# Kernel optimization log

Hardware: AMD Instinct MI355X
Metric: run time of the kernel (lower is better)

## Reference

```python
import jax, jax.numpy as jnp
import numpy as np

B, S, E = 2, 2048, 2048
H, KV, HD = 16, 4, 128  # num_heads, num_kv_heads, head_dim
G = H // KV             # query heads per kv head
ROPE_BASE = 10000.0


def rope_tables(dim, maxlen):
    freqs = 1.0 / ROPE_BASE ** (jnp.arange(0, dim, 2, dtype=jnp.float32) / dim)
    t = jnp.arange(maxlen, dtype=jnp.float32)
    f = jnp.outer(t, freqs)  # (maxlen, dim//2)
    return jnp.cos(f), jnp.sin(f)


def apply_rope(x, cos, sin):
    # x: (..., seq, heads, head_dim); interleaved-pair rotation
    s_len = x.shape[-3]
    c = cos[:s_len][:, None, :]
    s = sin[:s_len][:, None, :]
    x1 = x[..., ::2]
    x2 = x[..., 1::2]
    return jnp.stack([x1 * c - x2 * s, x1 * s + x2 * c], axis=-1).reshape(x.shape)


def setup_inputs() -> dict:
    key = jax.random.key(0)
    kx, kq, kk, kv, ko = jax.random.split(key, 5)
    x = jax.random.normal(kx, (B, S, E), dtype=jnp.float32)
    Wq = jax.random.normal(kq, (E, H * HD), dtype=jnp.float32) * 0.02
    Wk = jax.random.normal(kk, (E, KV * HD), dtype=jnp.float32) * 0.02
    Wv = jax.random.normal(kv, (E, KV * HD), dtype=jnp.float32) * 0.02
    Wo = jax.random.normal(ko, (H * HD, E), dtype=jnp.float32) * 0.02
    mask = jnp.tril(jnp.ones((S, S), dtype=bool))[None, None]  # causal (1,1,S,S)
    return {"x": x, "Wq": Wq, "Wk": Wk, "Wv": Wv, "Wo": Wo, "mask": mask}


def reference(x, Wq, Wk, Wv, Wo, mask):
    b, s, _ = x.shape
    cos, sin = rope_tables(HD, s)
    q = (x @ Wq).reshape(b, s, H, HD)
    k = (x @ Wk).reshape(b, s, KV, HD)
    v = (x @ Wv).reshape(b, s, KV, HD)
    q = apply_rope(q, cos, sin)
    k = apply_rope(k, cos, sin)
    if G > 1:
        k = jnp.repeat(k, G, axis=2)  # (b, s, H, HD)
        v = jnp.repeat(v, G, axis=2)
    q = jnp.transpose(q, (0, 2, 1, 3))  # (b, H, s, HD)
    k = jnp.transpose(k, (0, 2, 1, 3))
    v = jnp.transpose(v, (0, 2, 1, 3))
    scale = jnp.sqrt(jnp.float32(HD)).astype(q.dtype)
    scores = jnp.einsum("bhqd,bhkd->bhqk", q, k) / scale
    scores = jnp.where(mask, scores, jnp.finfo(scores.dtype).min)
    attn = jax.nn.softmax(scores, axis=-1)
    out = jnp.einsum("bhqk,bhkd->bhqd", attn, v)
    out = jnp.transpose(out, (0, 2, 1, 3)).reshape(b, s, H * HD)
    return out @ Wo
```

## Files before the change

### kernel.cpp

```cpp
#include <hip/hip_runtime.h>
#include <hip/hip_bf16.h>
#include <cstdint>

#define B_ 2
#define S_ 2048
#define E_ 2048
#define H_ 16
#define KV_ 4
#define HD_ 128
#define BS_ (B_*S_)
#define QKV_LD 3072
#define SM_SCALE 0.08838834764831845f

typedef __attribute__((ext_vector_type(8))) __bf16 bf16x8;
typedef __attribute__((ext_vector_type(4))) float  floatx4;

__device__ __forceinline__ unsigned short f2bf(float f) {
  union { float f; unsigned u; } v; v.f = f;
  unsigned r = v.u + 0x7fffu + ((v.u >> 16) & 1u);
  return (unsigned short)(r >> 16);
}
__device__ __forceinline__ float bf2f(unsigned short u) {
  union { unsigned u; float f; } v; v.u = ((unsigned)u) << 16; return v.f;
}

__global__ __launch_bounds__(256)
void cvt_bf16(const float* __restrict__ src, unsigned short* __restrict__ dst,
              int rows, int cols, int dld, int doff) {
  int idx = blockIdx.x * 256 + threadIdx.x;
  int n = rows * cols / 4;
  if (idx >= n) return;
  int e = idx * 4;
  int r = e / cols, c = e % cols;
  float4 v = *(const float4*)(src + (size_t)r * cols + c);
  ushort4 o;
  o.x = f2bf(v.x); o.y = f2bf(v.y); o.z = f2bf(v.z); o.w = f2bf(v.w);
  *(ushort4*)(dst + (size_t)r * dld + doff + c) = o;
}

__global__ __launch_bounds__(256)
void rope_kernel(unsigned short* __restrict__ qkv) {
  const int PPR = 1280;
  int idx = blockIdx.x * 256 + threadIdx.x;
  if (idx >= BS_ * PPR) return;
  int row = idx / PPR, p = idx - row * PPR;
  int col = (p < 1024) ? (2 * p) : (2048 + 2 * (p - 1024));
  int d = p & 63;
  int s = row & (S_ - 1);
  float freq = expf(-(float)d * 0.14391156831212787f);
  float ang = (float)s * freq;
  float c = cosf(ang), sn = sinf(ang);
  unsigned short* ptr = qkv + (size_t)row * QKV_LD + col;
  float x1 = bf2f(ptr[0]), x2 = bf2f(ptr[1]);
  ptr[0] = f2bf(x1 * c - x2 * sn);
  ptr[1] = f2bf(x1 * sn + x2 * c);
}

__global__ __launch_bounds__(256)
void vtrans_kernel(const unsigned short* __restrict__ qkv,
                   unsigned short* __restrict__ vt) {
  __shared__ unsigned short tile[64 * 72];
  const int tid = threadIdx.x;
  const int s0 = blockIdx.x * 64;
  const int g = blockIdx.y >> 1;
  const int hh = (blockIdx.y & 1) * 64;
  const int b = g >> 2, kvh = g & 3;
#pragma unroll
  for (int i = 0; i < 2; ++i) {
    int chunk = tid + i * 256;
    int r = chunk >> 3, c = (chunk & 7) * 8;
    uint4 v = *(const uint4*)(qkv + (size_t)(b * S_ + s0 + r) * QKV_LD + 2560 + kvh * HD_ + hh + c);
    *(uint4*)(tile + r * 72 + c) = v;
  }
  __syncthreads();
#pragma unroll
  for (int i = 0; i < 2; ++i) {
    int chunk = tid + i * 256;
    int hdr = chunk >> 3, sc = (chunk & 7) * 8;
    union { unsigned short u[8]; uint4 v; } t;
#pragma unroll
    for (int j = 0; j < 8; ++j) t.u[j] = tile[(sc + j) * 72 + hdr];
    *(uint4*)(vt + (size_t)(g * HD_ + hh + hdr) * S_ + s0 + sc) = t.v;
  }
}

template<bool OUT_BF16>
__global__ __launch_bounds__(256, 2)
void gemm_bf16(const unsigned short* __restrict__ A,
               const unsigned short* __restrict__ Bm,
               void* __restrict__ C, int M, int N, int K) {
  constexpr int ST = 72;
  __shared__ unsigned short Ash[128 * ST];
  __shared__ unsigned short Bt[128 * ST];
  const int tid = threadIdx.x;
  const int lane = tid & 63;
  const int l16 = lane & 15, l4 = lane >> 4;
  const int wave = tid >> 6;
  const int wm = (wave >> 1) * 64, wn = (wave & 1) * 64;
  const int bm = blockIdx.y * 128, bn = blockIdx.x * 128;

  floatx4 acc[4][4] = {};

  for (int kb = 0; kb < K; kb += 32) {
    __syncthreads();
#pragma unroll
    for (int i = 0; i < 2; ++i) {
      int chunk = tid + i * 256;
      int r = chunk >> 2, cc = (chunk & 3) * 8;
      uint4 v = *(const uint4*)(A + (size_t)(bm + r) * K + kb + cc);
      *(uint4*)(Ash + r * ST + cc) = v;
    }
#pragma unroll
    for (int i = 0; i < 2; ++i) {
      int chunk = tid + i * 256;
      int col = chunk & 127, kg = (chunk >> 7) * 8;
      const unsigned short* bp = Bm + (size_t)(kb + kg) * N + bn + col;
      union { unsigned short u[8]; uint4 v; } t;
#pragma unroll
      for (int j = 0; j < 8; ++j) t.u[j] = bp[(size_t)j * N];
      *(uint4*)(Bt + col * ST + kg) = t.v;
    }
    __syncthreads();
    bf16x8 af[4], bf[4];
#pragma unroll
    for (int t = 0; t < 4; ++t)
      af[t] = *(const bf16x8*)(Ash + (wm + t * 16 + l16) * ST + l4 * 8);
#pragma unroll
    for (int t = 0; t < 4; ++t)
      bf[t] = *(const bf16x8*)(Bt + (wn + t * 16 + l16) * ST + l4 * 8);
#pragma unroll
    for (int tm = 0; tm < 4; ++tm)
#pragma unroll
      for (int tn = 0; tn < 4; ++tn)
        acc[tm][tn] = __builtin_amdgcn_mfma_f32_16x16x32_bf16(af[tm], bf[tn], acc[tm][tn], 0, 0, 0);
  }
#pragma unroll
  for (int tm = 0; tm < 4; ++tm)
#pragma unroll
    for (int tn = 0; tn < 4; ++tn)
#pragma unroll
      for (int r = 0; r < 4; ++r) {
        int row = bm + wm + tm * 16 + l4 * 4 + r;
        int col = bn + wn + tn * 16 + l16;
        float v = acc[tm][tn][r];
        if (OUT_BF16) ((unsigned short*)C)[(size_t)row * N + col] = f2bf(v);
        else          ((float*)C)[(size_t)row * N + col] = v;
      }
}

__global__ __launch_bounds__(512, 2)
void gqa_attention(const unsigned short* __restrict__ qkv,
                   const unsigned short* __restrict__ vt,
                   unsigned short* __restrict__ out) {
  constexpr int KST = 136;
  constexpr int VST = 40;
  constexpr int PST = 40;
  __shared__ unsigned short Ksh[32 * KST];
  __shared__ unsigned short Vtsh[128 * VST];
  __shared__ unsigned short Psh[8][16 * PST];

  const int tid = threadIdx.x, lane = tid & 63, wave = tid >> 6;
  const int l16 = lane & 15, l4 = lane >> 4;
  const int g = blockIdx.y, b = g >> 2, kvh = g & 3;
  const int h = kvh * 4 + (wave & 3);
  const int qsub = wave >> 2;
  const int bx = blockIdx.x;

  const int kr = tid >> 4, kc = (tid & 15) * 8;
  const int vr = tid >> 2, vc = (tid & 3) * 8;

  for (int phase = 0; phase < 2; ++phase) {
    const int q0 = phase ? (S_ - 32 - bx * 32) : (bx * 32);
    const int qt = q0 + qsub * 16;

    bf16x8 qf[4];
    {
      const unsigned short* qp = qkv + (size_t)(b * S_ + qt + l16) * QKV_LD + h * HD_;
#pragma unroll
      for (int c = 0; c < 4; ++c)
        qf[c] = *(const bf16x8*)(qp + c * 32 + l4 * 8);
    }

    floatx4 acc[8] = {};
    float mrow[4], lrow[4];
#pragma unroll
    for (int r = 0; r < 4; ++r) { mrow[r] = -3e38f; lrow[r] = 0.f; }

    for (int kb = 0; kb <= q0; kb += 32) {
      __syncthreads();
      {
        uint4 v = *(const uint4*)(qkv + (size_t)(b * S_ + kb + kr) * QKV_LD + 2048 + kvh * HD_ + kc);
        *(uint4*)(Ksh + kr * KST + kc) = v;
      }
      {
        uint4 v = *(const uint4*)(vt + (size_t)(g * HD_ + vr) * S_ + kb + vc);
        *(uint4*)(Vtsh + vr * VST + vc) = v;
      }
      __syncthreads();

      floatx4 sacc[2] = {};
#pragma unroll
      for (int half = 0; half < 2; ++half)
#pragma unroll
        for (int c = 0; c < 4; ++c) {
          bf16x8 kf = *(const bf16x8*)(Ksh + (half * 16 + l16) * KST + c * 32 + l4 * 8);
          sacc[half] = __builtin_amdgcn_mfma_f32_16x16x32_bf16(qf[c], kf, sacc[half], 0, 0, 0);
        }
      float s[2][4];
      if (kb == q0) {
#pragma unroll
        for (int half = 0; half < 2; ++half)
#pragma unroll
          for (int r = 0; r < 4; ++r) {
            int ka = kb + half * 16 + l16;
            int qa = qt + l4 * 4 + r;
            s[half][r] = (ka > qa) ? -3e38f : sacc[half][r] * SM_SCALE;
          }
      } else {
#pragma unroll
        for (int half = 0; half < 2; ++half)
#pragma unroll
          for (int r = 0; r < 4; ++r)
            s[half][r] = sacc[half][r] * SM_SCALE;
      }
      float mx[4];
#pragma unroll
      for (int r = 0; r < 4; ++r) mx[r] = fmaxf(s[0][r], s[1][r]);
#pragma unroll
      for (int off = 1; off < 16; off <<= 1)
#pragma unroll
        for (int r = 0; r < 4; ++r)
          mx[r] = fmaxf(mx[r], __shfl_xor(mx[r], off, 64));
      float mnew[4], alpha[4], ps[4];
#pragma unroll
      for (int r = 0; r < 4; ++r) {
        mnew[r] = fmaxf(mrow[r], mx[r]);
        alpha[r] = __expf(mrow[r] - mnew[r]);
        ps[r] = 0.f;
      }
#pragma unroll
      for (int t = 0; t < 8; ++t)
#pragma unroll
        for (int r = 0; r < 4; ++r)
          acc[t][r] *= alpha[r];
#pragma unroll
      for (int half = 0; half < 2; ++half)
#pragma unroll
        for (int r = 0; r < 4; ++r) {
          float p = __expf(s[half][r] - mnew[r]);
          ps[r] += p;
          Psh[wave][(l4 * 4 + r) * PST + half * 16 + l16] = f2bf(p);
        }
#pragma unroll
      for (int off = 1; off < 16; off <<= 1)
#pragma unroll
        for (int r = 0; r < 4; ++r)
          ps[r] += __shfl_xor(ps[r], off, 64);
#pragma unroll
      for (int r = 0; r < 4; ++r) {
        lrow[r] = lrow[r] * alpha[r] + ps[r];
        mrow[r] = mnew[r];
      }
      bf16x8 pf = *(const bf16x8*)(&Psh[wave][l16 * PST + l4 * 8]);
#pragma unroll
      for (int t = 0; t < 8; ++t) {
        bf16x8 vf = *(const bf16x8*)(Vtsh + (t * 16 + l16) * VST + l4 * 8);
        acc[t] = __builtin_amdgcn_mfma_f32_16x16x32_bf16(pf, vf, acc[t], 0, 0, 0);
      }
    }
    float inv[4];
#pragma unroll
    for (int r = 0; r < 4; ++r) inv[r] = 1.0f / lrow[r];
#pragma unroll
    for (int t = 0; t < 8; ++t)
#pragma unroll
      for (int r = 0; r < 4; ++r) {
        int row = b * S_ + qt + l4 * 4 + r;
        int col = h * HD_ + t * 16 + l16;
        out[(size_t)row * 2048 + col] = f2bf(acc[t][r] * inv[r]);
      }
    __syncthreads();
  }
}

extern "C" void kernel_launch(void* const* d_in, const int* in_sizes, int n_in,
                              void* d_out, int out_size, void* d_ws, size_t ws_size,
                              hipStream_t stream) {
  const float* x  = (const float*)d_in[0];
  const float* Wq = (const float*)d_in[1];
  const float* Wk = (const float*)d_in[2];
  const float* Wv = (const float*)d_in[3];
  const float* Wo = (const float*)d_in[4];
  float* out = (float*)d_out;

  char* ws = (char*)d_ws;
  unsigned short* xb   = (unsigned short*)(ws);
  unsigned short* wqkv = (unsigned short*)(ws + 16777216);
  unsigned short* wo   = (unsigned short*)(ws + 29360128);
  unsigned short* qkv  = (unsigned short*)(ws + 37748736);
  unsigned short* attn = (unsigned short*)(ws + 62914560);
  unsigned short* vt   = (unsigned short*)(ws);

  {
    int n = 4096 * 2048 / 4;
    cvt_bf16<<<(n + 255) / 256, 256, 0, stream>>>(x, xb, 4096, 2048, 2048, 0);
  }
  {
    int n = 2048 * 2048 / 4;
    cvt_bf16<<<(n + 255) / 256, 256, 0, stream>>>(Wq, wqkv, 2048, 2048, 3072, 0);
  }
  {
    int n = 2048 * 512 / 4;
    cvt_bf16<<<(n + 255) / 256, 256, 0, stream>>>(Wk, wqkv, 2048, 512, 3072, 2048);
    cvt_bf16<<<(n + 255) / 256, 256, 0, stream>>>(Wv, wqkv, 2048, 512, 3072, 2560);
  }
  {
    int n = 2048 * 2048 / 4;
    cvt_bf16<<<(n + 255) / 256, 256, 0, stream>>>(Wo, wo, 2048, 2048, 2048, 0);
  }

  gemm_bf16<true><<<dim3(3072 / 128, 4096 / 128), 256, 0, stream>>>(xb, wqkv, qkv, 4096, 3072, 2048);
  rope_kernel<<<(4096 * 1280 + 255) / 256, 256, 0, stream>>>(qkv);
  vtrans_kernel<<<dim3(32, 16), 256, 0, stream>>>(qkv, vt);
  gqa_attention<<<dim3(32, 8), 512, 0, stream>>>(qkv, vt, attn);
  gemm_bf16<false><<<dim3(2048 / 128, 4096 / 128), 256, 0, stream>>>(attn, wo, out, 4096, 2048, 2048);
}
```

Baseline: 410.0 us.

## Transpose weights at conversion, use async LDS loads and double-buffered attention

```diff
diff --git a/kernel.cpp b/kernel.cpp
--- a/kernel.cpp
+++ b/kernel.cpp
@@ -24,18 +24,46 @@
   union { unsigned u; float f; } v; v.u = ((unsigned)u) << 16; return v.f;
 }
 
+__device__ __forceinline__ void async_cp16(const void* g, void* l) {
+  __builtin_amdgcn_global_load_lds(
+      (const __attribute__((address_space(1))) void*)g,
+      (__attribute__((address_space(3))) void*)l, 16, 0, 0);
+}
+
 __global__ __launch_bounds__(256)
 void cvt_bf16(const float* __restrict__ src, unsigned short* __restrict__ dst,
-              int rows, int cols, int dld, int doff) {
+              int n4) {
   int idx = blockIdx.x * 256 + threadIdx.x;
-  int n = rows * cols / 4;
-  if (idx >= n) return;
-  int e = idx * 4;
-  int r = e / cols, c = e % cols;
-  float4 v = *(const float4*)(src + (size_t)r * cols + c);
+  if (idx >= n4) return;
+  float4 v = *(const float4*)(src + (size_t)idx * 4);
   ushort4 o;
   o.x = f2bf(v.x); o.y = f2bf(v.y); o.z = f2bf(v.z); o.w = f2bf(v.w);
-  *(ushort4*)(dst + (size_t)r * dld + doff + c) = o;
+  *(ushort4*)(dst + (size_t)idx * 4) = o;
+}
+
+__global__ __launch_bounds__(256)
+void cvt_bf16_t(const float* __restrict__ src, unsigned short* __restrict__ dst,
+                int N, int dld, int noff) {
+  __shared__ float tile[64 * 65];
+  const int t = threadIdx.x;
+  const int bk = blockIdx.y * 64, bn = blockIdx.x * 64;
+  const int r = t >> 2, cg = t & 3;
+#pragma unroll
+  for (int i = 0; i < 4; ++i) {
+    int c = cg * 16 + i * 4;
+    float4 v = *(const float4*)(src + (size_t)(bk + r) * N + bn + c);
+    tile[r * 65 + c] = v.x; tile[r * 65 + c + 1] = v.y;
+    tile[r * 65 + c + 2] = v.z; tile[r * 65 + c + 3] = v.w;
+  }
+  __syncthreads();
+  const int nl = t >> 2, kg = t & 3;
+  union { unsigned short u[16]; uint4 q[2]; } o;
+#pragma unroll
+  for (int j = 0; j < 16; ++j)
+    o.u[j] = f2bf(tile[(kg * 16 + j) * 65 + nl]);
+  unsigned short* dp = dst + (size_t)(noff + bn + nl) * dld + bk + kg * 16;
+  *(uint4*)(dp) = o.q[0];
+  *(uint4*)(dp + 8) = o.q[1];
 }
 
 __global__ __launch_bounds__(256)
@@ -86,48 +114,45 @@
 
 template<bool OUT_BF16>
 __global__ __launch_bounds__(256, 2)
-void gemm_bf16(const unsigned short* __restrict__ A,
-               const unsigned short* __restrict__ Bm,
-               void* __restrict__ C, int M, int N, int K) {
-  constexpr int ST = 72;
-  __shared__ unsigned short Ash[128 * ST];
-  __shared__ unsigned short Bt[128 * ST];
+void gemm_tn(const unsigned short* __restrict__ A,
+             const unsigned short* __restrict__ BT,
+             void* __restrict__ C, int M, int N, int K) {
+  __shared__ unsigned short Ash[128 * 32];
+  __shared__ unsigned short Bsh[128 * 32];
   const int tid = threadIdx.x;
-  const int lane = tid & 63;
-  const int l16 = lane & 15, l4 = lane >> 4;
+  const int l = tid & 63;
+  const int l16 = l & 15, l4 = l >> 4;
   const int wave = tid >> 6;
   const int wm = (wave >> 1) * 64, wn = (wave & 1) * 64;
   const int bm = blockIdx.y * 128, bn = blockIdx.x * 128;
 
+  const int srow = l >> 2;
+  const int sg = (((l & 3) - (l >> 4)) & 3) * 8;
+
   floatx4 acc[4][4] = {};
 
   for (int kb = 0; kb < K; kb += 32) {
     __syncthreads();
 #pragma unroll
     for (int i = 0; i < 2; ++i) {
-      int chunk = tid + i * 256;
-      int r = chunk >> 2, cc = (chunk & 3) * 8;
-      uint4 v = *(const uint4*)(A + (size_t)(bm + r) * K + kb + cc);
-      *(uint4*)(Ash + r * ST + cc) = v;
-    }
-#pragma unroll
-    for (int i = 0; i < 2; ++i) {
-      int chunk = tid + i * 256;
-      int col = chunk & 127, kg = (chunk >> 7) * 8;
-      const unsigned short* bp = Bm + (size_t)(kb + kg) * N + bn + col;
-      union { unsigned short u[8]; uint4 v; } t;
-#pragma unroll
-      for (int j = 0; j < 8; ++j) t.u[j] = bp[(size_t)j * N];
-      *(uint4*)(Bt + col * ST + kg) = t.v;
+      int cc = wave + i * 4;
+      async_cp16(A + (size_t)(bm + 16 * cc + srow) * K + kb + sg, &Ash[cc * 512]);
+      async_cp16(BT + (size_t)(bn + 16 * cc + srow) * K + kb + sg, &Bsh[cc * 512]);
     }
     __syncthreads();
     bf16x8 af[4], bf[4];
 #pragma unroll
-    for (int t = 0; t < 4; ++t)
-      af[t] = *(const bf16x8*)(Ash + (wm + t * 16 + l16) * ST + l4 * 8);
-#pragma unroll
-    for (int t = 0; t < 4; ++t)
-      bf[t] = *(const bf16x8*)(Bt + (wn + t * 16 + l16) * ST + l4 * 8);
+    for (int t = 0; t < 4; ++t) {
+      int row = wm + t * 16 + l16;
+      int s = (l4 + (l16 >> 2)) & 3;
+      af[t] = *(const bf16x8*)(Ash + row * 32 + s * 8);
+    }
+#pragma unroll
+    for (int t = 0; t < 4; ++t) {
+      int row = wn + t * 16 + l16;
+      int s = (l4 + (l16 >> 2)) & 3;
+      bf[t] = *(const bf16x8*)(Bsh + row * 32 + s * 8);
+    }
 #pragma unroll
     for (int tm = 0; tm < 4; ++tm)
 #pragma unroll
@@ -148,30 +173,27 @@
       }
 }
 
-__global__ __launch_bounds__(512, 2)
+__global__ __launch_bounds__(256, 2)
 void gqa_attention(const unsigned short* __restrict__ qkv,
                    const unsigned short* __restrict__ vt,
                    unsigned short* __restrict__ out) {
-  constexpr int KST = 136;
-  constexpr int VST = 40;
-  constexpr int PST = 40;
-  __shared__ unsigned short Ksh[32 * KST];
-  __shared__ unsigned short Vtsh[128 * VST];
-  __shared__ unsigned short Psh[8][16 * PST];
-
-  const int tid = threadIdx.x, lane = tid & 63, wave = tid >> 6;
-  const int l16 = lane & 15, l4 = lane >> 4;
+  __shared__ unsigned short Ksh[2][32 * 128];
+  __shared__ unsigned short Vsh[2][128 * 32];
+  __shared__ unsigned short Psh[4][16 * 40];
+
+  const int tid = threadIdx.x, l = tid & 63, wave = tid >> 6;
+  const int l16 = l & 15, l4 = l >> 4;
   const int g = blockIdx.y, b = g >> 2, kvh = g & 3;
-  const int h = kvh * 4 + (wave & 3);
-  const int qsub = wave >> 2;
+  const int h = kvh * 4 + wave;
   const int bx = blockIdx.x;
 
-  const int kr = tid >> 4, kc = (tid & 15) * 8;
-  const int vr = tid >> 2, vc = (tid & 3) * 8;
+  const int k_subrow = l >> 4;
+  const int v_subrow = l >> 2;
+  const int v_g = (((l & 3) - (l >> 4)) & 3) * 8;
 
   for (int phase = 0; phase < 2; ++phase) {
-    const int q0 = phase ? (S_ - 32 - bx * 32) : (bx * 32);
-    const int qt = q0 + qsub * 16;
+    const int qt = phase ? (S_ - 16 - bx * 16) : (bx * 16);
+    const int nch = ((qt + 15) >> 5) + 1;
 
     bf16x8 qf[4];
     {
@@ -180,106 +202,112 @@
       for (int c = 0; c < 4; ++c)
         qf[c] = *(const bf16x8*)(qp + c * 32 + l4 * 8);
     }
-
+    asm volatile("s_waitcnt vmcnt(0)" ::: "memory");
+
+    {
+      const int kb = 0;
+#pragma unroll
+      for (int i = 0; i < 2; ++i) {
+        int cc = wave + i * 4;
+        int gk = (((l & 15) - 4 * cc - k_subrow) & 15) * 8;
+        async_cp16(qkv + (size_t)(b * S_ + kb + 4 * cc + k_subrow) * QKV_LD + 2048 + kvh * HD_ + gk,
+                   &Ksh[0][cc * 512]);
+        async_cp16(vt + (size_t)(g * HD_ + 16 * cc + v_subrow) * S_ + kb + v_g,
+                   &Vsh[0][cc * 512]);
+      }
+    }
+
+    float m = -3e38f, lsum = 0.f;
     floatx4 acc[8] = {};
-    float mrow[4], lrow[4];
-#pragma unroll
-    for (int r = 0; r < 4; ++r) { mrow[r] = -3e38f; lrow[r] = 0.f; }
-
-    for (int kb = 0; kb <= q0; kb += 32) {
-      __syncthreads();
+
+    for (int it = 0; it < nch; ++it) {
+      const int kb = it * 32;
+      const int cur = it & 1;
+      asm volatile("s_barrier" ::: "memory");
       {
-        uint4 v = *(const uint4*)(qkv + (size_t)(b * S_ + kb + kr) * QKV_LD + 2048 + kvh * HD_ + kc);
-        *(uint4*)(Ksh + kr * KST + kc) = v;
-      }
-      {
-        uint4 v = *(const uint4*)(vt + (size_t)(g * HD_ + vr) * S_ + kb + vc);
-        *(uint4*)(Vtsh + vr * VST + vc) = v;
-      }
-      __syncthreads();
+        const int kb2 = (it + 1 < nch) ? kb + 32 : 0;
+#pragma unroll
+        for (int i = 0; i < 2; ++i) {
+          int cc = wave + i * 4;
+          int gk = (((l & 15) - 4 * cc - k_subrow) & 15) * 8;
+          async_cp16(qkv + (size_t)(b * S_ + kb2 + 4 * cc + k_subrow) * QKV_LD + 2048 + kvh * HD_ + gk,
+                     &Ksh[cur ^ 1][cc * 512]);
+          async_cp16(vt + (size_t)(g * HD_ + 16 * cc + v_subrow) * S_ + kb2 + v_g,
+                     &Vsh[cur ^ 1][cc * 512]);
+        }
+      }
+      asm volatile("s_waitcnt vmcnt(4)\n\ts_barrier" ::: "memory");
 
       floatx4 sacc[2] = {};
 #pragma unroll
+      for (int half = 0; half < 2; ++half) {
+        int krow = half * 16 + l16;
+#pragma unroll
+        for (int c = 0; c < 4; ++c) {
+          int s = (c * 4 + l4 + l16) & 15;
+          bf16x8 kf = *(const bf16x8*)(&Ksh[cur][krow * 128 + s * 8]);
+          sacc[half] = __builtin_amdgcn_mfma_f32_16x16x32_bf16(kf, qf[c], sacc[half], 0, 0, 0);
+        }
+      }
+      float sv[8];
+      const bool need_mask = (kb + 31 > qt);
+#pragma unroll
       for (int half = 0; half < 2; ++half)
 #pragma unroll
-        for (int c = 0; c < 4; ++c) {
-          bf16x8 kf = *(const bf16x8*)(Ksh + (half * 16 + l16) * KST + c * 32 + l4 * 8);
-          sacc[half] = __builtin_amdgcn_mfma_f32_16x16x32_bf16(qf[c], kf, sacc[half], 0, 0, 0);
+        for (int r = 0; r < 4; ++r) {
+          float v = sacc[half][r] * SM_SCALE;
+          if (need_mask) {
+            int ka = kb + half * 16 + l4 * 4 + r;
+            if (ka > qt + l16) v = -3e38f;
+          }
+          sv[half * 4 + r] = v;
         }
-      float s[2][4];
-      if (kb == q0) {
-#pragma unroll
-        for (int half = 0; half < 2; ++half)
-#pragma unroll
-          for (int r = 0; r < 4; ++r) {
-            int ka = kb + half * 16 + l16;
-            int qa = qt + l4 * 4 + r;
-            s[half][r] = (ka > qa) ? -3e38f : sacc[half][r] * SM_SCALE;
-          }
-      } else {
-#pragma unroll
-        for (int half = 0; half < 2; ++half)
-#pragma unroll
-          for (int r = 0; r < 4; ++r)
-            s[half][r] = sacc[half][r] * SM_SCALE;
-      }
-      float mx[4];
-#pragma unroll
-      for (int r = 0; r < 4; ++r) mx[r] = fmaxf(s[0][r], s[1][r]);
-#pragma unroll
-      for (int off = 1; off < 16; off <<= 1)
+      float mx = sv[0];
+#pragma unroll
+      for (int j = 1; j < 8; ++j) mx = fmaxf(mx, sv[j]);
+      mx = fmaxf(mx, __shfl_xor(mx, 16, 64));
+      mx = fmaxf(mx, __shfl_xor(mx, 32, 64));
+      float mnew = fmaxf(m, mx);
+      float alpha = __expf(m - mnew);
+      float p[8], psum = 0.f;
+#pragma unroll
+      for (int j = 0; j < 8; ++j) { p[j] = __expf(sv[j] - mnew); psum += p[j]; }
+      psum += __shfl_xor(psum, 16, 64);
+      psum += __shfl_xor(psum, 32, 64);
+      lsum = lsum * alpha + psum;
+      m = mnew;
+#pragma unroll
+      for (int t = 0; t < 8; ++t)
 #pragma unroll
         for (int r = 0; r < 4; ++r)
-          mx[r] = fmaxf(mx[r], __shfl_xor(mx[r], off, 64));
-      float mnew[4], alpha[4], ps[4];
-#pragma unroll
-      for (int r = 0; r < 4; ++r) {
-        mnew[r] = fmaxf(mrow[r], mx[r]);
-        alpha[r] = __expf(mrow[r] - mnew[r]);
-        ps[r] = 0.f;
-      }
-#pragma unroll
-      for (int t = 0; t < 8; ++t)
-#pragma unroll
-        for (int r = 0; r < 4; ++r)
-          acc[t][r] *= alpha[r];
-#pragma unroll
-      for (int half = 0; half < 2; ++half)
-#pragma unroll
-        for (int r = 0; r < 4; ++r) {
-          float p = __expf(s[half][r] - mnew[r]);
-          ps[r] += p;
-          Psh[wave][(l4 * 4 + r) * PST + half * 16 + l16] = f2bf(p);
-        }
-#pragma unroll
-      for (int off = 1; off < 16; off <<= 1)
-#pragma unroll
-        for (int r = 0; r < 4; ++r)
-          ps[r] += __shfl_xor(ps[r], off, 64);
-#pragma unroll
-      for (int r = 0; r < 4; ++r) {
-        lrow[r] = lrow[r] * alpha[r] + ps[r];
-        mrow[r] = mnew[r];
-      }
-      bf16x8 pf = *(const bf16x8*)(&Psh[wave][l16 * PST + l4 * 8]);
+          acc[t][r] *= alpha;
+#pragma unroll
+      for (int half = 0; half < 2; ++half) {
+        ushort4 pk;
+        pk.x = f2bf(p[half * 4 + 0]); pk.y = f2bf(p[half * 4 + 1]);
+        pk.z = f2bf(p[half * 4 + 2]); pk.w = f2bf(p[half * 4 + 3]);
+        *(ushort4*)(&Psh[wave][l16 * 40 + half * 16 + l4 * 4]) = pk;
+      }
+      bf16x8 pf = *(const bf16x8*)(&Psh[wave][l16 * 40 + l4 * 8]);
 #pragma unroll
       for (int t = 0; t < 8; ++t) {
-        bf16x8 vf = *(const bf16x8*)(Vtsh + (t * 16 + l16) * VST + l4 * 8);
-        acc[t] = __builtin_amdgcn_mfma_f32_16x16x32_bf16(pf, vf, acc[t], 0, 0, 0);
-      }
-    }
-    float inv[4];
-#pragma unroll
-    for (int r = 0; r < 4; ++r) inv[r] = 1.0f / lrow[r];
-#pragma unroll
-    for (int t = 0; t < 8; ++t)
-#pragma unroll
-      for (int r = 0; r < 4; ++r) {
-        int row = b * S_ + qt + l4 * 4 + r;
-        int col = h * HD_ + t * 16 + l16;
-        out[(size_t)row * 2048 + col] = f2bf(acc[t][r] * inv[r]);
-      }
-    __syncthreads();
+        int row = t * 16 + l16;
+        int s = (l4 + (l16 >> 2)) & 3;
+        bf16x8 vf = *(const bf16x8*)(&Vsh[cur][row * 32 + s * 8]);
+        acc[t] = __builtin_amdgcn_mfma_f32_16x16x32_bf16(vf, pf, acc[t], 0, 0, 0);
+      }
+    }
+    asm volatile("s_barrier" ::: "memory");
+
+    float inv = 1.0f / lsum;
+    unsigned short* op = out + (size_t)(b * S_ + qt + l16) * 2048 + h * HD_;
+#pragma unroll
+    for (int t = 0; t < 8; ++t) {
+      ushort4 o;
+      o.x = f2bf(acc[t][0] * inv); o.y = f2bf(acc[t][1] * inv);
+      o.z = f2bf(acc[t][2] * inv); o.w = f2bf(acc[t][3] * inv);
+      *(ushort4*)(op + t * 16 + l4 * 4) = o;
+    }
   }
 }
 
@@ -294,34 +322,22 @@
   float* out = (float*)d_out;
 
   char* ws = (char*)d_ws;
-  unsigned short* xb   = (unsigned short*)(ws);
-  unsigned short* wqkv = (unsigned short*)(ws + 16777216);
-  unsigned short* wo   = (unsigned short*)(ws + 29360128);
-  unsigned short* qkv  = (unsigned short*)(ws + 37748736);
-  unsigned short* attn = (unsigned short*)(ws + 62914560);
-  unsigned short* vt   = (unsigned short*)(ws);
-
-  {
-    int n = 4096 * 2048 / 4;
-    cvt_bf16<<<(n + 255) / 256, 256, 0, stream>>>(x, xb, 4096, 2048, 2048, 0);
-  }
-  {
-    int n = 2048 * 2048 / 4;
-    cvt_bf16<<<(n + 255) / 256, 256, 0, stream>>>(Wq, wqkv, 2048, 2048, 3072, 0);
-  }
-  {
-    int n = 2048 * 512 / 4;
-    cvt_bf16<<<(n + 255) / 256, 256, 0, stream>>>(Wk, wqkv, 2048, 512, 3072, 2048);
-    cvt_bf16<<<(n + 255) / 256, 256, 0, stream>>>(Wv, wqkv, 2048, 512, 3072, 2560);
-  }
-  {
-    int n = 2048 * 2048 / 4;
-    cvt_bf16<<<(n + 255) / 256, 256, 0, stream>>>(Wo, wo, 2048, 2048, 2048, 0);
-  }
-
-  gemm_bf16<true><<<dim3(3072 / 128, 4096 / 128), 256, 0, stream>>>(xb, wqkv, qkv, 4096, 3072, 2048);
+  unsigned short* xb    = (unsigned short*)(ws);
+  unsigned short* wqkvT = (unsigned short*)(ws + 16777216);
+  unsigned short* woT   = (unsigned short*)(ws + 29360128);
+  unsigned short* qkv   = (unsigned short*)(ws + 37748736);
+  unsigned short* attn  = (unsigned short*)(ws + 62914560);
+  unsigned short* vt    = (unsigned short*)(ws);
+
+  cvt_bf16<<<(4096 * 2048 / 4 + 255) / 256, 256, 0, stream>>>(x, xb, 4096 * 2048 / 4);
+  cvt_bf16_t<<<dim3(32, 32), 256, 0, stream>>>(Wq, wqkvT, 2048, 2048, 0);
+  cvt_bf16_t<<<dim3(8, 32),  256, 0, stream>>>(Wk, wqkvT, 512,  2048, 2048);
+  cvt_bf16_t<<<dim3(8, 32),  256, 0, stream>>>(Wv, wqkvT, 512,  2048, 2560);
+  cvt_bf16_t<<<dim3(32, 32), 256, 0, stream>>>(Wo, woT,  2048, 2048, 0);
+
+  gemm_tn<true><<<dim3(24, 32), 256, 0, stream>>>(xb, wqkvT, qkv, 4096, 3072, 2048);
   rope_kernel<<<(4096 * 1280 + 255) / 256, 256, 0, stream>>>(qkv);
   vtrans_kernel<<<dim3(32, 16), 256, 0, stream>>>(qkv, vt);
-  gqa_attention<<<dim3(32, 8), 512, 0, stream>>>(qkv, vt, attn);
-  gemm_bf16<false><<<dim3(2048 / 128, 4096 / 128), 256, 0, stream>>>(attn, wo, out, 4096, 2048, 2048);
-}
+  gqa_attention<<<dim3(64, 8), 256, 0, stream>>>(qkv, vt, attn);
+  gemm_tn<false><<<dim3(16, 32), 256, 0, stream>>>(attn, woT, out, 4096, 2048, 2048);
+}
```

Result: faster. 365.6 us (-10.8%).
